# Performance work log

Hardware: AMD Instinct MI355X
Metric: run time of the kernel (lower is better)

## Reference

```python
import math
import jax, jax.numpy as jnp
import numpy as np

HID = 2048      # hidden_size
NH = 16         # num_heads
KD = HID // NH  # key head dim = 128 (even, required by XPOS)
VD = HID        # value_dim (value_factor=1)
VHD = VD // NH  # value head dim
SCALE_BASE = 512
ROPE_BASE = 10000.0
GN_EPS = 1e-5


def _rotate_every_two(x):
    x1 = x[..., ::2]
    x2 = x[..., 1::2]
    return jnp.stack((-x2, x1), axis=-1).reshape(x.shape)


def _dup(a):  # repeat_interleave(x, 2, dim=-1)
    return jnp.repeat(a, 2, axis=-1)


def _xpos_apply(x, pos, inv_freq, xpos_scale, downscale):
    # x: [B, H, S, KD], pos: [B, S]
    posf = pos.astype(jnp.float32)
    angles = posf[:, :, None] * inv_freq[None, None, :]          # [B, S, KD/2]
    sin = _dup(jnp.sin(angles))[:, None]                          # [B, 1, S, KD]
    cos = _dup(jnp.cos(angles))[:, None]
    scale = xpos_scale[None, None, :] ** (posf[:, :, None] / SCALE_BASE)
    if downscale:
        scale = 1.0 / scale
    scale = _dup(scale)[:, None]                                  # [B, 1, S, KD]
    return (x * cos + _rotate_every_two(x) * sin) * scale


def setup_inputs() -> dict:
    key = jax.random.key(0)
    ks = jax.random.split(key, 6)
    B, S = 1, 2048
    std = 1.0 / HID
    x = jax.random.normal(ks[0], (B, S, HID), dtype=jnp.float32)
    position_ids = jnp.broadcast_to(jnp.arange(S, dtype=jnp.int64), (B, S))
    Wq = jax.random.normal(ks[1], (HID, HID), dtype=jnp.float32) * std
    Wk = jax.random.normal(ks[2], (HID, HID), dtype=jnp.float32) * std
    Wv = jax.random.normal(ks[3], (HID, VD), dtype=jnp.float32) * std
    Wg = jax.random.normal(ks[4], (HID, VD), dtype=jnp.float32) * std
    Wo = jax.random.normal(ks[5], (VD, HID), dtype=jnp.float32) * std
    gn_weight = jnp.ones((VD,), dtype=jnp.float32)
    gn_bias = jnp.zeros((VD,), dtype=jnp.float32)
    return {"x": x, "position_ids": position_ids, "Wq": Wq, "Wk": Wk,
            "Wv": Wv, "Wg": Wg, "Wo": Wo,
            "gn_weight": gn_weight, "gn_bias": gn_bias}


def reference(x, position_ids, Wq, Wk, Wv, Wg, Wo, gn_weight, gn_bias):
    B, S, _ = x.shape
    # XPOS / multiscale-decay buffers (deterministic, as in XPOSRelativePosition)
    inv_freq = 1.0 / (ROPE_BASE ** (jnp.arange(0, KD, 2, dtype=jnp.float32) / KD))
    xpos_scale = (jnp.arange(0, KD, 2, dtype=jnp.float32) + 0.4 * KD) / (1.4 * KD)
    gamma = 1.0 - jnp.exp(jnp.linspace(math.log(1.0 / 32), math.log(1.0 / 512), NH))
    log_gamma = jnp.log(gamma)                                    # [NH]

    # projections -> [B, H, S, d]
    q = (x @ Wq).reshape(B, S, NH, KD).transpose(0, 2, 1, 3)
    k = (x @ Wk).reshape(B, S, NH, KD).transpose(0, 2, 1, 3)
    v = (x @ Wv).reshape(B, S, NH, VHD).transpose(0, 2, 1, 3)
    g = x @ Wg                                                    # [B, S, VD]

    q = _xpos_apply(q, position_ids, inv_freq, xpos_scale, downscale=False)
    k = _xpos_apply(k, position_ids, inv_freq, xpos_scale, downscale=True)

    # decay mask: exp(log_gamma * (i-j)) for i>=j else 0   [B, H, S, S]
    relpos = position_ids[:, :, None] - position_ids[:, None, :]  # [B, S, S]
    decay = jnp.exp(log_gamma[None, :, None, None]
                    * jnp.maximum(relpos, 0)[:, None].astype(jnp.float32))
    decay = decay * (relpos >= 0)[:, None].astype(jnp.float32)

    scores = jnp.einsum('bhqd,bhkd->bhqk', q, k) * decay          # [B, H, S, S]
    retained = jnp.einsum('bhqk,bhkv->bhqv', scores, v)           # [B, H, S, VHD]

    # GroupNorm(num_heads, value_dim): normalize each head group per token
    r = retained.transpose(0, 2, 1, 3)                            # [B, S, H, VHD]
    mean = r.mean(axis=-1, keepdims=True)
    var = r.var(axis=-1, keepdims=True)
    rn = (r - mean) * jax.lax.rsqrt(var + GN_EPS)
    rn = rn * gn_weight.reshape(NH, VHD) + gn_bias.reshape(NH, VHD)
    rn = rn.reshape(B, S, VD)

    out = (jax.nn.silu(g) * rn) @ Wo                              # [B, S, HID]
    return out
```

## Files before the change

kernel.cpp:

```cpp
#include <hip/hip_runtime.h>
#include <math.h>

#define S_LEN 2048
#define HIDD  2048
#define NHEAD 16
#define HD    128

#define TILE_SH 4096

typedef __attribute__((ext_vector_type(8))) short short8;
typedef __attribute__((ext_vector_type(4))) float float4v;
typedef unsigned short ushort_t;

static __device__ __forceinline__ ushort_t f2bf(float f) {
    unsigned int u = __float_as_uint(f);
    u += 0x7fff + ((u >> 16) & 1);
    return (ushort_t)(u >> 16);
}
static __device__ __forceinline__ float bf2f(ushort_t s) {
    return __uint_as_float(((unsigned int)s) << 16);
}
__device__ __forceinline__ float silu_f(float x) { return x / (1.f + expf(-x)); }

__device__ __forceinline__ void gl_lds16(const ushort_t* g, short* l) {
    __builtin_amdgcn_global_load_lds((const __attribute__((address_space(1))) void*)g,
                                     (__attribute__((address_space(3))) void*)l, 16, 0, 0);
}

__global__ __launch_bounds__(256)
void split_kernel(const float* __restrict__ in, ushort_t* __restrict__ hi,
                  ushort_t* __restrict__ lo, int n4)
{
    const int i = blockIdx.x * 256 + threadIdx.x;
    if (i >= n4) return;
    const float4 v = ((const float4*)in)[i];
    ushort4 h, l;
    h.x = f2bf(v.x); l.x = f2bf(v.x - bf2f(h.x));
    h.y = f2bf(v.y); l.y = f2bf(v.y - bf2f(h.y));
    h.z = f2bf(v.z); l.z = f2bf(v.z - bf2f(h.z));
    h.w = f2bf(v.w); l.w = f2bf(v.w - bf2f(h.w));
    const int row = i >> 9, c4 = (i & 511) * 4;
    const size_t off = ((size_t)((row >> 7) * 64 + (c4 >> 5))) * TILE_SH
                     + (row & 127) * 32 + (c4 & 31);
    *(ushort4*)&hi[off] = h;
    *(ushort4*)&lo[off] = l;
}

__global__ __launch_bounds__(256)
void addp_kernel(float* __restrict__ out, const float* __restrict__ p, int n4)
{
    const int i = blockIdx.x * 256 + threadIdx.x;
    if (i >= n4) return;
    float4 a = ((const float4*)out)[i];
    const float4 b = ((const float4*)p)[i];
    a.x += b.x; a.y += b.y; a.z += b.z; a.w += b.w;
    ((float4*)out)[i] = a;
}

__global__ __launch_bounds__(256)
void split_transpose(const float* __restrict__ W, ushort_t* __restrict__ Thi,
                     ushort_t* __restrict__ Tlo)
{
    __shared__ float t[64][65];
    const int k0 = blockIdx.y * 64, n0 = blockIdx.x * 64;
    const int tx = threadIdx.x & 15, ty = threadIdx.x >> 4;
    #pragma unroll
    for (int it = 0; it < 4; it++) {
        const int k = ty + it * 16;
        const float4 v = *(const float4*)&W[(size_t)(k0 + k) * HIDD + n0 + tx * 4];
        t[k][tx * 4 + 0] = v.x; t[k][tx * 4 + 1] = v.y;
        t[k][tx * 4 + 2] = v.z; t[k][tx * 4 + 3] = v.w;
    }
    __syncthreads();
    #pragma unroll
    for (int it = 0; it < 4; it++) {
        const int n = ty + it * 16;
        ushort4 h, l; float a;
        a = t[tx * 4 + 0][n]; h.x = f2bf(a); l.x = f2bf(a - bf2f(h.x));
        a = t[tx * 4 + 1][n]; h.y = f2bf(a); l.y = f2bf(a - bf2f(h.y));
        a = t[tx * 4 + 2][n]; h.z = f2bf(a); l.z = f2bf(a - bf2f(h.z));
        a = t[tx * 4 + 3][n]; h.w = f2bf(a); l.w = f2bf(a - bf2f(h.w));
        const int nn_ = n0 + n, kk_ = k0 + tx * 4;
        const size_t off = ((size_t)((nn_ >> 7) * 64 + (kk_ >> 5))) * TILE_SH
                         + (nn_ & 127) * 32 + (kk_ & 31);
        *(ushort4*)&Thi[off] = h;
        *(ushort4*)&Tlo[off] = l;
    }
}

template<int MODE>
__global__ __launch_bounds__(256, 2)
void mfma_gemm(const ushort_t* __restrict__ Ahi, const ushort_t* __restrict__ Alo,
               const ushort_t* __restrict__ WT, const int* __restrict__ pos_ids,
               ushort_t* __restrict__ qhi, ushort_t* __restrict__ qlo,
               ushort_t* __restrict__ khi, ushort_t* __restrict__ klo,
               ushort_t* __restrict__ vThi, ushort_t* __restrict__ vTlo,
               float* __restrict__ gbuf, float* __restrict__ outC)
{
    __shared__ __align__(16) short sm[32768];

    const int tid = threadIdx.x;
    const int w = tid >> 6, L = tid & 63;
    const int qd = L >> 4, lc = L & 15;
    const int lin = blockIdx.x;
    int n0, m0, kh = 0;
    if (MODE == 0) {
        n0 = (((lin & 7) << 3) + ((lin >> 3) & 7)) << 7;
        m0 = (lin >> 6) << 7;
    } else {
        n0 = (lin & 15) << 7;
        m0 = ((lin >> 4) & 15) << 7;
        kh = lin >> 8;
    }
    const size_t PL = (size_t)HIDD * HIDD;

    int sel, nn;
    const ushort_t *Bhi, *Blo;
    if (MODE == 0) {
        sel = n0 >> 11; nn = n0 & 2047;
        Bhi = WT + (size_t)sel * 2 * PL; Blo = Bhi + PL;
    } else {
        sel = -1; nn = n0;
        Bhi = WT; Blo = WT + PL;
    }

    const ushort_t* pbase = (w == 0) ? Ahi : (w == 1) ? Alo : (w == 2) ? Bhi : Blo;
    const int rt = ((w < 2) ? m0 : nn) >> 7;
    const int lsw = ((L >> 2) * 32) + (((L & 3) ^ ((L >> 2) & 3)) * 8);
    const ushort_t* tb0 = pbase + (size_t)rt * 64 * TILE_SH + lsw;

    const int wm = (w & 1) * 64, wn = (w >> 1) * 64;
    const int sx = (qd ^ (lc & 3)) * 8;
    int aoff[4], boff[4];
    #pragma unroll
    for (int i = 0; i < 4; i++) aoff[i] = (wm + i * 16 + lc) * 32 + sx;
    #pragma unroll
    for (int j = 0; j < 4; j++) boff[j] = (wn + j * 16 + lc) * 32 + sx;

    float4v acc[4][4];
    #pragma unroll
    for (int i = 0; i < 4; i++)
        #pragma unroll
        for (int j = 0; j < 4; j++)
            #pragma unroll
            for (int r = 0; r < 4; r++) acc[i][j][r] = 0.f;

    const int kt0 = (MODE == 1) ? kh * 32 : 0;
    const int kt1 = (MODE == 1) ? kt0 + 32 : 64;

    {
        const ushort_t* g = tb0 + (size_t)kt0 * TILE_SH;
        #pragma unroll
        for (int t = 0; t < 8; t++)
            gl_lds16(g + t * 512, sm + w * 4096 + t * 512);
        asm volatile("s_waitcnt vmcnt(0)" ::: "memory");
        __builtin_amdgcn_s_barrier();
        __builtin_amdgcn_sched_barrier(0);
    }

    int cur = 0;
    for (int kt = kt0; kt < kt1; kt++) {
        const short* cb = sm + (cur << 14);
        short* nb = sm + ((cur ^ 1) << 14);
        if (kt + 1 < kt1) {
            const ushort_t* g = tb0 + (size_t)(kt + 1) * TILE_SH;
            #pragma unroll
            for (int t = 0; t < 8; t++)
                gl_lds16(g + t * 512, nb + w * 4096 + t * 512);
        }

        short8 bhf[4], blf[4];
        #pragma unroll
        for (int j = 0; j < 4; j++) {
            bhf[j] = *(const short8*)(cb + 8192  + boff[j]);
            blf[j] = *(const short8*)(cb + 12288 + boff[j]);
        }
        #pragma unroll
        for (int i = 0; i < 4; i++) {
            const short8 ahf = *(const short8*)(cb + aoff[i]);
            const short8 alf = *(const short8*)(cb + 4096 + aoff[i]);
            #pragma unroll
            for (int j = 0; j < 4; j++) {
                acc[i][j] = __builtin_amdgcn_mfma_f32_16x16x32_bf16(ahf, bhf[j], acc[i][j], 0, 0, 0);
                acc[i][j] = __builtin_amdgcn_mfma_f32_16x16x32_bf16(alf, bhf[j], acc[i][j], 0, 0, 0);
                acc[i][j] = __builtin_amdgcn_mfma_f32_16x16x32_bf16(ahf, blf[j], acc[i][j], 0, 0, 0);
            }
        }

        asm volatile("s_waitcnt vmcnt(0)" ::: "memory");
        __builtin_amdgcn_s_barrier();
        __builtin_amdgcn_sched_barrier(0);
        cur ^= 1;
    }

    float* ob = (float*)sm;
    const int half = w & 1;
    const int head = nn >> 7;

    #pragma unroll
    for (int i = 0; i < 4; i++) {
        #pragma unroll
        for (int j = 0; j < 4; j++)
            #pragma unroll
            for (int r = 0; r < 4; r++)
                ob[(half * 16 + qd * 4 + r) * 132 + wn + j * 16 + lc] = acc[i][j][r];
        __syncthreads();

        if (MODE == 1 || sel == 3) {
            float* dst = (MODE == 1) ? (kh ? gbuf : outC) : gbuf;
            #pragma unroll
            for (int p = 0; p < 4; p++) {
                const int row = p * 8 + (tid >> 5);
                const int c = (tid & 31) * 4;
                const int grow = m0 + (row >> 4) * 64 + i * 16 + (row & 15);
                const float4 vv = *(const float4*)&ob[row * 132 + c];
                *(float4*)&dst[(size_t)grow * HIDD + nn + c] = vv;
            }
        } else if (sel == 2) {
            const int d = tid >> 1, hs = tid & 1;
            const int sbase = m0 + hs * 64 + i * 16;
            short8 h0, h1, l0, l1;
            #pragma unroll
            for (int sp = 0; sp < 8; sp++) {
                float a = ob[(hs * 16 + sp) * 132 + d];
                ushort_t hb = f2bf(a);
                h0[sp] = (short)hb; l0[sp] = (short)f2bf(a - bf2f(hb));
                a = ob[(hs * 16 + 8 + sp) * 132 + d];
                hb = f2bf(a);
                h1[sp] = (short)hb; l1[sp] = (short)f2bf(a - bf2f(hb));
            }
            ushort_t* dh = vThi + ((size_t)head * HD + d) * S_LEN + sbase;
            ushort_t* dl = vTlo + ((size_t)head * HD + d) * S_LEN + sbase;
            *(short8*)dh = h0; *(short8*)(dh + 8) = h1;
            *(short8*)dl = l0; *(short8*)(dl + 8) = l1;
        } else {
            const float sgn = (sel == 0) ? 1.f : -1.f;
            ushort_t* dhb = (sel == 0) ? qhi : khi;
            ushort_t* dlb = (sel == 0) ? qlo : klo;
            #pragma unroll
            for (int p = 0; p < 2; p++) {
                const int row = p * 16 + (tid >> 4);
                const int c8 = (tid & 15) * 8;
                const int grow = m0 + (row >> 4) * 64 + i * 16 + (row & 15);
                const float pos = (float)pos_ids[grow];
                const float pe = sgn * pos * (1.f / 512.f);
                short8 hv, lv;
                #pragma unroll
                for (int pp = 0; pp < 4; pp++) {
                    const int d = c8 + pp * 2;
                    const float v0 = ob[row * 132 + d], v1 = ob[row * 132 + d + 1];
                    const float invf = exp2f(-(float)d * (13.28771238f / 128.f));
                    float s, c_; sincosf(pos * invf, &s, &c_);
                    const float scl = exp2f(log2f(((float)d + 51.2f) * (1.f / 179.2f)) * pe);
                    const float e0 = (v0 * c_ - v1 * s) * scl;
                    const float e1 = (v1 * c_ + v0 * s) * scl;
                    const ushort_t h0 = f2bf(e0), h1 = f2bf(e1);
                    hv[pp * 2] = (short)h0;  hv[pp * 2 + 1] = (short)h1;
                    lv[pp * 2] = (short)f2bf(e0 - bf2f(h0));
                    lv[pp * 2 + 1] = (short)f2bf(e1 - bf2f(h1));
                }
                *(short8*)&dhb[((size_t)head * S_LEN + grow) * HD + c8] = hv;
                *(short8*)&dlb[((size_t)head * S_LEN + grow) * HD + c8] = lv;
            }
        }
        __syncthreads();
    }
}

#define KROW 136
#define VROW 40
#define KH_  0
#define KL_  (32 * KROW)
#define VH_  (2 * 32 * KROW)
#define VL_  (VH_ + 128 * VROW)
#define PH_  (VH_ + 2 * 128 * VROW)
#define PLO_ (PH_ + 64 * VROW)
#define YH_  8704
#define YL_  (YH_ + 64 * KROW)
__global__ __launch_bounds__(256, 2)
void retention2(const ushort_t* __restrict__ qhi, const ushort_t* __restrict__ qlo,
                const ushort_t* __restrict__ khi, const ushort_t* __restrict__ klo,
                const ushort_t* __restrict__ vThi, const ushort_t* __restrict__ vTlo,
                const float* __restrict__ gbuf, const float* __restrict__ gnw,
                const float* __restrict__ gnb,
                ushort_t* __restrict__ yhi, ushort_t* __restrict__ ylo)
{
    __shared__ __align__(16) short sm[26112];

    const int h = blockIdx.y;
    const int qb = (gridDim.x - 1) - blockIdx.x;
    const int r0 = qb * 64;
    const int tid = threadIdx.x;
    const int w = tid >> 6, L = tid & 63;
    const int qd = L >> 4, lc = L & 15;

    const float e = -3.4657359f + (float)h * ((-6.2383246f + 3.4657359f) / 15.f);
    const float lg2g = logf(1.f - expf(e)) * 1.44269504f;

    short8 qfh[4], qfl[4];
    {
        const size_t qb0 = ((size_t)h * S_LEN + r0 + w * 16 + lc) * HD + qd * 8;
        #pragma unroll
        for (int ks = 0; ks < 4; ks++) {
            qfh[ks] = *(const short8*)(qhi + qb0 + ks * 32);
            qfl[ks] = *(const short8*)(qlo + qb0 + ks * 32);
        }
    }

    float4v osum[2][4];
    #pragma unroll
    for (int mt = 0; mt < 2; mt++)
        #pragma unroll
        for (int j = 0; j < 4; j++)
            #pragma unroll
            for (int r = 0; r < 4; r++) osum[mt][j][r] = 0.f;

    const int qh_ = w >> 1, vh_ = w & 1;
    const int nch = (r0 + 64) / 32;

    for (int ch = 0; ch < nch; ch++) {
        const int kg0 = ch * 32;
        #pragma unroll
        for (int t = 0; t < 4; t++) {
            const int c = t * 256 + tid;
            const int p = c >> 9, r = (c >> 4) & 31, qq = c & 15;
            const ushort_t* src = (p ? klo : khi) + ((size_t)h * S_LEN + kg0 + r) * HD + qq * 8;
            *(short8*)(sm + (p ? KL_ : KH_) + r * KROW + qq * 8) = *(const short8*)src;
        }
        #pragma unroll
        for (int t = 0; t < 4; t++) {
            const int c = t * 256 + tid;
            const int p = c >> 9, r = (c >> 2) & 127, qq = c & 3;
            const ushort_t* src = (p ? vTlo : vThi) + ((size_t)h * HD + r) * S_LEN + kg0 + qq * 8;
            *(short8*)(sm + (p ? VL_ : VH_) + r * VROW + qq * 8) = *(const short8*)src;
        }
        __syncthreads();

        float4v sacc[2];
        #pragma unroll
        for (int j = 0; j < 2; j++)
            #pragma unroll
            for (int r = 0; r < 4; r++) sacc[j][r] = 0.f;
        #pragma unroll
        for (int ks = 0; ks < 4; ks++) {
            #pragma unroll
            for (int j = 0; j < 2; j++) {
                const short8 bh = *(const short8*)(sm + KH_ + (j * 16 + lc) * KROW + ks * 32 + qd * 8);
                const short8 bl = *(const short8*)(sm + KL_ + (j * 16 + lc) * KROW + ks * 32 + qd * 8);
                sacc[j] = __builtin_amdgcn_mfma_f32_16x16x32_bf16(qfh[ks], bh, sacc[j], 0, 0, 0);
                sacc[j] = __builtin_amdgcn_mfma_f32_16x16x32_bf16(qfl[ks], bh, sacc[j], 0, 0, 0);
                sacc[j] = __builtin_amdgcn_mfma_f32_16x16x32_bf16(qfh[ks], bl, sacc[j], 0, 0, 0);
            }
        }
        #pragma unroll
        for (int j = 0; j < 2; j++)
            #pragma unroll
            for (int r = 0; r < 4; r++) {
                const int dq = (r0 + w * 16 + qd * 4 + r) - (kg0 + j * 16 + lc);
                const float p = (dq >= 0) ? sacc[j][r] * exp2f(lg2g * (float)dq) : 0.f;
                const ushort_t hb = f2bf(p);
                const int off = (w * 16 + qd * 4 + r) * VROW + j * 16 + lc;
                sm[PH_ + off]  = (short)hb;
                sm[PLO_ + off] = (short)f2bf(p - bf2f(hb));
            }
        __syncthreads();

        #pragma unroll
        for (int mt = 0; mt < 2; mt++) {
            const short8 pfh = *(const short8*)(sm + PH_  + (qh_ * 32 + mt * 16 + lc) * VROW + qd * 8);
            const short8 pfl = *(const short8*)(sm + PLO_ + (qh_ * 32 + mt * 16 + lc) * VROW + qd * 8);
            #pragma unroll
            for (int j = 0; j < 4; j++) {
                const short8 vfh = *(const short8*)(sm + VH_ + (vh_ * 64 + j * 16 + lc) * VROW + qd * 8);
                const short8 vfl = *(const short8*)(sm + VL_ + (vh_ * 64 + j * 16 + lc) * VROW + qd * 8);
                osum[mt][j] = __builtin_amdgcn_mfma_f32_16x16x32_bf16(pfh, vfh, osum[mt][j], 0, 0, 0);
                osum[mt][j] = __builtin_amdgcn_mfma_f32_16x16x32_bf16(pfl, vfh, osum[mt][j], 0, 0, 0);
                osum[mt][j] = __builtin_amdgcn_mfma_f32_16x16x32_bf16(pfh, vfl, osum[mt][j], 0, 0, 0);
            }
        }
        __syncthreads();
    }

    float* fr = (float*)sm;
    #pragma unroll
    for (int mt = 0; mt < 2; mt++)
        #pragma unroll
        for (int r = 0; r < 4; r++) {
            float s1 = 0.f, s2 = 0.f;
            #pragma unroll
            for (int j = 0; j < 4; j++) { const float v = osum[mt][j][r]; s1 += v; s2 += v * v; }
            const int row = qh_ * 32 + mt * 16 + qd * 4 + r;
            fr[row * 32 + vh_ * 16 + lc] = s1;
            fr[2048 + row * 32 + vh_ * 16 + lc] = s2;
        }
    __syncthreads();
    if (tid < 64) {
        float s1 = 0.f, s2 = 0.f;
        #pragma unroll
        for (int t = 0; t < 32; t++) { s1 += fr[tid * 32 + t]; s2 += fr[2048 + tid * 32 + t]; }
        const float mean = s1 * (1.f / 128.f);
        const float var  = s2 * (1.f / 128.f) - mean * mean;
        fr[4096 + tid] = mean;
        fr[4160 + tid] = 1.f / sqrtf(var + 1e-5f);
    }
    __syncthreads();

    #pragma unroll
    for (int mt = 0; mt < 2; mt++)
        #pragma unroll
        for (int r = 0; r < 4; r++) {
            const int row = qh_ * 32 + mt * 16 + qd * 4 + r;
            const float mean = fr[4096 + row], inv = fr[4160 + row];
            const int grow = r0 + row;
            #pragma unroll
            for (int j = 0; j < 4; j++) {
                const int col = vh_ * 64 + j * 16 + lc;
                const float gv = gbuf[(size_t)grow * HIDD + h * HD + col];
                const float o = ((osum[mt][j][r] - mean) * inv * gnw[h * HD + col]
                                 + gnb[h * HD + col]) * silu_f(gv);
                const ushort_t hb = f2bf(o);
                sm[YH_ + row * KROW + col] = (short)hb;
                sm[YL_ + row * KROW + col] = (short)f2bf(o - bf2f(hb));
            }
        }
    __syncthreads();
    {
        const int r_ = tid >> 2, cs = (tid & 3) * 32;
        const int grow = r0 + r_;
        const size_t tb = ((size_t)((grow >> 7) * 64 + h * 4 + (tid & 3))) * TILE_SH
                        + (grow & 127) * 32;
        #pragma unroll
        for (int c8 = 0; c8 < 4; c8++) {
            *(short8*)(yhi + tb + c8 * 8) = *(const short8*)(sm + YH_ + r_ * KROW + cs + c8 * 8);
            *(short8*)(ylo + tb + c8 * 8) = *(const short8*)(sm + YL_ + r_ * KROW + cs + c8 * 8);
        }
    }
}

extern "C" void kernel_launch(void* const* d_in, const int* in_sizes, int n_in,
                              void* d_out, int out_size, void* d_ws, size_t ws_size,
                              hipStream_t stream) {
    const float* x   = (const float*)d_in[0];
    const int*   pid = (const int*)d_in[1];
    const float* W[5] = {(const float*)d_in[2], (const float*)d_in[3], (const float*)d_in[4],
                         (const float*)d_in[5], (const float*)d_in[6]};
    const float* gnw = (const float*)d_in[7];
    const float* gnb = (const float*)d_in[8];
    float* out = (float*)d_out;
    (void)in_sizes; (void)n_in; (void)out_size; (void)ws_size;

    const size_t PL = (size_t)HIDD * HIDD;

    ushort_t* wt   = (ushort_t*)d_ws;
    ushort_t* xhi  = wt + 10 * PL;
    ushort_t* xlo  = xhi + PL;
    ushort_t* qhi_ = xlo + PL;
    ushort_t* qlo_ = qhi_ + PL;
    ushort_t* khi_ = qlo_ + PL;
    ushort_t* klo_ = khi_ + PL;
    ushort_t* vThi = klo_ + PL;
    ushort_t* vTlo = vThi + PL;
    float*    gbuf = (float*)(vTlo + PL);
    ushort_t* yhi  = (ushort_t*)(gbuf + PL);
    ushort_t* ylo  = yhi + PL;
    float*    p1   = (float*)xhi;

    split_kernel<<<(int)(PL / 4 / 256), 256, 0, stream>>>(x, xhi, xlo, (int)(PL / 4));
    for (int m = 0; m < 5; m++)
        split_transpose<<<dim3(32, 32), 256, 0, stream>>>(W[m], wt + (size_t)m * 2 * PL,
                                                          wt + (size_t)m * 2 * PL + PL);

    mfma_gemm<0><<<1024, 256, 0, stream>>>(xhi, xlo, wt, pid,
        qhi_, qlo_, khi_, klo_, vThi, vTlo, gbuf, nullptr);

    retention2<<<dim3(32, 16), 256, 0, stream>>>(qhi_, qlo_, khi_, klo_, vThi, vTlo,
        gbuf, gnw, gnb, yhi, ylo);

    mfma_gemm<1><<<512, 256, 0, stream>>>(yhi, ylo, wt + 8 * PL, pid,
        nullptr, nullptr, nullptr, nullptr, nullptr, nullptr, p1, out);

    addp_kernel<<<(int)(PL / 4 / 256), 256, 0, stream>>>(out, p1, (int)(PL / 4));
}
```

Before: 535.5 us.

## Widen GEMM tiles to 128x256 and split output GEMM K four ways

The split-bf16 MFMA GEMM now computes 128x256 output tiles per block instead of 128x128, so each A tile loaded into LDS is reused across twice as many columns. The grid drops to 512 blocks for both GEMMs, and the output projection splits K into four parts instead of two to keep the block count. The extra partials are summed by an extended add kernel. The A-side load is reordered after a barrier so it can reuse a single buffer, which trades some copy overlap and more LDS and registers (32 accumulators) for fewer redundant loads.

```diff
diff --git a/kernel.cpp b/kernel.cpp
--- a/kernel.cpp
+++ b/kernel.cpp
@@ -52,8 +52,13 @@
     const int i = blockIdx.x * 256 + threadIdx.x;
     if (i >= n4) return;
     float4 a = ((const float4*)out)[i];
-    const float4 b = ((const float4*)p)[i];
-    a.x += b.x; a.y += b.y; a.z += b.z; a.w += b.w;
+    const float4 b0 = ((const float4*)p)[i];
+    const float4 b1 = ((const float4*)p)[i + n4];
+    const float4 b2 = ((const float4*)p)[i + 2 * n4];
+    a.x += b0.x + b1.x + b2.x;
+    a.y += b0.y + b1.y + b2.y;
+    a.z += b0.z + b1.z + b2.z;
+    a.w += b0.w + b1.w + b2.w;
     ((float4*)out)[i] = a;
 }
 
@@ -97,7 +102,7 @@
                ushort_t* __restrict__ vThi, ushort_t* __restrict__ vTlo,
                float* __restrict__ gbuf, float* __restrict__ outC)
 {
-    __shared__ __align__(16) short sm[32768];
+    __shared__ __align__(16) short sm[40960];
 
     const int tid = threadIdx.x;
     const int w = tid >> 6, L = tid & 63;
@@ -105,12 +110,12 @@
     const int lin = blockIdx.x;
     int n0, m0, kh = 0;
     if (MODE == 0) {
-        n0 = (((lin & 7) << 3) + ((lin >> 3) & 7)) << 7;
-        m0 = (lin >> 6) << 7;
+        n0 = (((lin & 7) << 2) + ((lin >> 3) & 3)) << 8;
+        m0 = (lin >> 5) << 7;
     } else {
-        n0 = (lin & 15) << 7;
-        m0 = ((lin >> 4) & 15) << 7;
-        kh = lin >> 8;
+        n0 = (lin & 7) << 8;
+        m0 = ((lin >> 3) & 15) << 7;
+        kh = lin >> 7;
     }
     const size_t PL = (size_t)HIDD * HIDD;
 
@@ -126,33 +131,40 @@
 
     const ushort_t* pbase = (w == 0) ? Ahi : (w == 1) ? Alo : (w == 2) ? Bhi : Blo;
     const int rt = ((w < 2) ? m0 : nn) >> 7;
-    const int lsw = ((L >> 2) * 32) + (((L & 3) ^ ((L >> 2) & 3)) * 8);
-    const ushort_t* tb0 = pbase + (size_t)rt * 64 * TILE_SH + lsw;
-
-    const int wm = (w & 1) * 64, wn = (w >> 1) * 64;
-    const int sx = (qd ^ (lc & 3)) * 8;
-    int aoff[4], boff[4];
-    #pragma unroll
-    for (int i = 0; i < 4; i++) aoff[i] = (wm + i * 16 + lc) * 32 + sx;
-    #pragma unroll
-    for (int j = 0; j < 4; j++) boff[j] = (wn + j * 16 + lc) * 32 + sx;
-
-    float4v acc[4][4];
+    const ushort_t* tb0 = pbase + (size_t)rt * 64 * TILE_SH + L * 8;
+
+    const int wm = (w & 1) * 64;
+    const int wnh = w >> 1;
+    int aoff[4], boff[8];
+    #pragma unroll
+    for (int i = 0; i < 4; i++) aoff[i] = (wm + i * 16 + lc) * 32 + qd * 8;
+    #pragma unroll
+    for (int jj = 0; jj < 8; jj++) boff[jj] = (jj * 16 + lc) * 32 + qd * 8;
+
+    float4v acc[4][8];
     #pragma unroll
     for (int i = 0; i < 4; i++)
         #pragma unroll
-        for (int j = 0; j < 4; j++)
-            #pragma unroll
-            for (int r = 0; r < 4; r++) acc[i][j][r] = 0.f;
-
-    const int kt0 = (MODE == 1) ? kh * 32 : 0;
-    const int kt1 = (MODE == 1) ? kt0 + 32 : 64;
+        for (int jj = 0; jj < 8; jj++)
+            #pragma unroll
+            for (int r = 0; r < 4; r++) acc[i][jj][r] = 0.f;
+
+    const int kt0 = (MODE == 1) ? kh * 16 : 0;
+    const int kt1 = (MODE == 1) ? kt0 + 16 : 64;
 
     {
         const ushort_t* g = tb0 + (size_t)kt0 * TILE_SH;
-        #pragma unroll
-        for (int t = 0; t < 8; t++)
-            gl_lds16(g + t * 512, sm + w * 4096 + t * 512);
+        if (w < 2) {
+            short* d = sm + w * 4096;
+            #pragma unroll
+            for (int t = 0; t < 8; t++) gl_lds16(g + t * 512, d + t * 512);
+        } else {
+            short* d = sm + 8192 + (w - 2) * 8192;
+            #pragma unroll
+            for (int t = 0; t < 8; t++) gl_lds16(g + t * 512, d + t * 512);
+            #pragma unroll
+            for (int t = 0; t < 8; t++) gl_lds16(g + 64 * TILE_SH + t * 512, d + 4096 + t * 512);
+        }
         asm volatile("s_waitcnt vmcnt(0)" ::: "memory");
         __builtin_amdgcn_s_barrier();
         __builtin_amdgcn_sched_barrier(0);
@@ -160,33 +172,49 @@
 
     int cur = 0;
     for (int kt = kt0; kt < kt1; kt++) {
-        const short* cb = sm + (cur << 14);
-        short* nb = sm + ((cur ^ 1) << 14);
-        if (kt + 1 < kt1) {
+        if (w >= 2 && kt + 1 < kt1) {
             const ushort_t* g = tb0 + (size_t)(kt + 1) * TILE_SH;
-            #pragma unroll
-            for (int t = 0; t < 8; t++)
-                gl_lds16(g + t * 512, nb + w * 4096 + t * 512);
-        }
-
-        short8 bhf[4], blf[4];
-        #pragma unroll
-        for (int j = 0; j < 4; j++) {
-            bhf[j] = *(const short8*)(cb + 8192  + boff[j]);
-            blf[j] = *(const short8*)(cb + 12288 + boff[j]);
-        }
+            short* d = sm + 8192 + ((cur ^ 1) * 16384) + (w - 2) * 8192;
+            #pragma unroll
+            for (int t = 0; t < 8; t++) gl_lds16(g + t * 512, d + t * 512);
+            #pragma unroll
+            for (int t = 0; t < 8; t++) gl_lds16(g + 64 * TILE_SH + t * 512, d + 4096 + t * 512);
+        }
+
+        short8 ah[4], al[4];
         #pragma unroll
         for (int i = 0; i < 4; i++) {
-            const short8 ahf = *(const short8*)(cb + aoff[i]);
-            const short8 alf = *(const short8*)(cb + 4096 + aoff[i]);
+            ah[i] = *(const short8*)(sm + aoff[i]);
+            al[i] = *(const short8*)(sm + 4096 + aoff[i]);
+        }
+        const short* bb = sm + 8192 + cur * 16384 + wnh * 4096;
+        #pragma unroll
+        for (int jh = 0; jh < 2; jh++) {
+            short8 bh[4], bl[4];
             #pragma unroll
             for (int j = 0; j < 4; j++) {
-                acc[i][j] = __builtin_amdgcn_mfma_f32_16x16x32_bf16(ahf, bhf[j], acc[i][j], 0, 0, 0);
-                acc[i][j] = __builtin_amdgcn_mfma_f32_16x16x32_bf16(alf, bhf[j], acc[i][j], 0, 0, 0);
-                acc[i][j] = __builtin_amdgcn_mfma_f32_16x16x32_bf16(ahf, blf[j], acc[i][j], 0, 0, 0);
-            }
-        }
-
+                bh[j] = *(const short8*)(bb + boff[jh * 4 + j]);
+                bl[j] = *(const short8*)(bb + 8192 + boff[jh * 4 + j]);
+            }
+            #pragma unroll
+            for (int i = 0; i < 4; i++)
+                #pragma unroll
+                for (int j = 0; j < 4; j++) {
+                    acc[i][jh * 4 + j] = __builtin_amdgcn_mfma_f32_16x16x32_bf16(ah[i], bh[j], acc[i][jh * 4 + j], 0, 0, 0);
+                    acc[i][jh * 4 + j] = __builtin_amdgcn_mfma_f32_16x16x32_bf16(al[i], bh[j], acc[i][jh * 4 + j], 0, 0, 0);
+                    acc[i][jh * 4 + j] = __builtin_amdgcn_mfma_f32_16x16x32_bf16(ah[i], bl[j], acc[i][jh * 4 + j], 0, 0, 0);
+                }
+        }
+
+        asm volatile("s_waitcnt lgkmcnt(0)" ::: "memory");
+        __builtin_amdgcn_s_barrier();
+        __builtin_amdgcn_sched_barrier(0);
+        if (w < 2 && kt + 1 < kt1) {
+            const ushort_t* g = tb0 + (size_t)(kt + 1) * TILE_SH;
+            short* d = sm + w * 4096;
+            #pragma unroll
+            for (int t = 0; t < 8; t++) gl_lds16(g + t * 512, d + t * 512);
+        }
         asm volatile("s_waitcnt vmcnt(0)" ::: "memory");
         __builtin_amdgcn_s_barrier();
         __builtin_amdgcn_sched_barrier(0);
@@ -194,73 +222,82 @@
     }
 
     float* ob = (float*)sm;
-    const int half = w & 1;
-    const int head = nn >> 7;
+    const int mh = w & 1;
+    const int headb = nn >> 7;
 
     #pragma unroll
     for (int i = 0; i < 4; i++) {
         #pragma unroll
-        for (int j = 0; j < 4; j++)
+        for (int jj = 0; jj < 8; jj++)
             #pragma unroll
             for (int r = 0; r < 4; r++)
-                ob[(half * 16 + qd * 4 + r) * 132 + wn + j * 16 + lc] = acc[i][j][r];
+                ob[(mh * 16 + qd * 4 + r) * 260 + wnh * 128 + jj * 16 + lc] = acc[i][jj][r];
         __syncthreads();
 
         if (MODE == 1 || sel == 3) {
-            float* dst = (MODE == 1) ? (kh ? gbuf : outC) : gbuf;
-            #pragma unroll
-            for (int p = 0; p < 4; p++) {
-                const int row = p * 8 + (tid >> 5);
-                const int c = (tid & 31) * 4;
+            float* dst = (MODE == 1) ? ((kh == 0) ? outC : gbuf + (size_t)(kh - 1) * PL)
+                                     : gbuf;
+            #pragma unroll
+            for (int p = 0; p < 8; p++) {
+                const int row = p * 4 + (tid >> 6);
+                const int c = (tid & 63) * 4;
                 const int grow = m0 + (row >> 4) * 64 + i * 16 + (row & 15);
-                const float4 vv = *(const float4*)&ob[row * 132 + c];
+                const float4 vv = *(const float4*)&ob[row * 260 + c];
                 *(float4*)&dst[(size_t)grow * HIDD + nn + c] = vv;
             }
         } else if (sel == 2) {
             const int d = tid >> 1, hs = tid & 1;
             const int sbase = m0 + hs * 64 + i * 16;
-            short8 h0, h1, l0, l1;
-            #pragma unroll
-            for (int sp = 0; sp < 8; sp++) {
-                float a = ob[(hs * 16 + sp) * 132 + d];
-                ushort_t hb = f2bf(a);
-                h0[sp] = (short)hb; l0[sp] = (short)f2bf(a - bf2f(hb));
-                a = ob[(hs * 16 + 8 + sp) * 132 + d];
-                hb = f2bf(a);
-                h1[sp] = (short)hb; l1[sp] = (short)f2bf(a - bf2f(hb));
-            }
-            ushort_t* dh = vThi + ((size_t)head * HD + d) * S_LEN + sbase;
-            ushort_t* dl = vTlo + ((size_t)head * HD + d) * S_LEN + sbase;
-            *(short8*)dh = h0; *(short8*)(dh + 8) = h1;
-            *(short8*)dl = l0; *(short8*)(dl + 8) = l1;
+            #pragma unroll
+            for (int nh = 0; nh < 2; nh++) {
+                short8 h0, h1, l0, l1;
+                #pragma unroll
+                for (int sp = 0; sp < 8; sp++) {
+                    float a = ob[(hs * 16 + sp) * 260 + nh * 128 + d];
+                    ushort_t hb = f2bf(a);
+                    h0[sp] = (short)hb; l0[sp] = (short)f2bf(a - bf2f(hb));
+                    a = ob[(hs * 16 + 8 + sp) * 260 + nh * 128 + d];
+                    hb = f2bf(a);
+                    h1[sp] = (short)hb; l1[sp] = (short)f2bf(a - bf2f(hb));
+                }
+                ushort_t* dh = vThi + ((size_t)(headb + nh) * HD + d) * S_LEN + sbase;
+                ushort_t* dl = vTlo + ((size_t)(headb + nh) * HD + d) * S_LEN + sbase;
+                *(short8*)dh = h0; *(short8*)(dh + 8) = h1;
+                *(short8*)dl = l0; *(short8*)(dl + 8) = l1;
+            }
         } else {
             const float sgn = (sel == 0) ? 1.f : -1.f;
             ushort_t* dhb = (sel == 0) ? qhi : khi;
             ushort_t* dlb = (sel == 0) ? qlo : klo;
             #pragma unroll
-            for (int p = 0; p < 2; p++) {
-                const int row = p * 16 + (tid >> 4);
-                const int c8 = (tid & 15) * 8;
-                const int grow = m0 + (row >> 4) * 64 + i * 16 + (row & 15);
-                const float pos = (float)pos_ids[grow];
-                const float pe = sgn * pos * (1.f / 512.f);
-                short8 hv, lv;
+            for (int nh = 0; nh < 2; nh++) {
+                const int head = headb + nh;
                 #pragma unroll
-                for (int pp = 0; pp < 4; pp++) {
-                    const int d = c8 + pp * 2;
-                    const float v0 = ob[row * 132 + d], v1 = ob[row * 132 + d + 1];
-                    const float invf = exp2f(-(float)d * (13.28771238f / 128.f));
-                    float s, c_; sincosf(pos * invf, &s, &c_);
-                    const float scl = exp2f(log2f(((float)d + 51.2f) * (1.f / 179.2f)) * pe);
-                    const float e0 = (v0 * c_ - v1 * s) * scl;
-                    const float e1 = (v1 * c_ + v0 * s) * scl;
-                    const ushort_t h0 = f2bf(e0), h1 = f2bf(e1);
-                    hv[pp * 2] = (short)h0;  hv[pp * 2 + 1] = (short)h1;
-                    lv[pp * 2] = (short)f2bf(e0 - bf2f(h0));
-                    lv[pp * 2 + 1] = (short)f2bf(e1 - bf2f(h1));
+                for (int p = 0; p < 2; p++) {
+                    const int row = p * 16 + (tid >> 4);
+                    const int c8 = (tid & 15) * 8;
+                    const int grow = m0 + (row >> 4) * 64 + i * 16 + (row & 15);
+                    const float pos = (float)pos_ids[grow];
+                    const float pe = sgn * pos * (1.f / 512.f);
+                    short8 hv, lv;
+                    #pragma unroll
+                    for (int pp = 0; pp < 4; pp++) {
+                        const int d = c8 + pp * 2;
+                        const float v0 = ob[row * 260 + nh * 128 + d];
+                        const float v1 = ob[row * 260 + nh * 128 + d + 1];
+                        const float invf = exp2f(-(float)d * (13.28771238f / 128.f));
+                        float s, c_; sincosf(pos * invf, &s, &c_);
+                        const float scl = exp2f(log2f(((float)d + 51.2f) * (1.f / 179.2f)) * pe);
+                        const float e0 = (v0 * c_ - v1 * s) * scl;
+                        const float e1 = (v1 * c_ + v0 * s) * scl;
+                        const ushort_t h0 = f2bf(e0), h1 = f2bf(e1);
+                        hv[pp * 2] = (short)h0;  hv[pp * 2 + 1] = (short)h1;
+                        lv[pp * 2] = (short)f2bf(e0 - bf2f(h0));
+                        lv[pp * 2 + 1] = (short)f2bf(e1 - bf2f(h1));
+                    }
+                    *(short8*)&dhb[((size_t)head * S_LEN + grow) * HD + c8] = hv;
+                    *(short8*)&dlb[((size_t)head * S_LEN + grow) * HD + c8] = lv;
                 }
-                *(short8*)&dhb[((size_t)head * S_LEN + grow) * HD + c8] = hv;
-                *(short8*)&dlb[((size_t)head * S_LEN + grow) * HD + c8] = lv;
             }
         }
         __syncthreads();
@@ -463,21 +500,21 @@
     float*    gbuf = (float*)(vTlo + PL);
     ushort_t* yhi  = (ushort_t*)(gbuf + PL);
     ushort_t* ylo  = yhi + PL;
-    float*    p1   = (float*)xhi;
+    float*    pb   = (float*)xhi;
 
     split_kernel<<<(int)(PL / 4 / 256), 256, 0, stream>>>(x, xhi, xlo, (int)(PL / 4));
     for (int m = 0; m < 5; m++)
         split_transpose<<<dim3(32, 32), 256, 0, stream>>>(W[m], wt + (size_t)m * 2 * PL,
                                                           wt + (size_t)m * 2 * PL + PL);
 
-    mfma_gemm<0><<<1024, 256, 0, stream>>>(xhi, xlo, wt, pid,
+    mfma_gemm<0><<<512, 256, 0, stream>>>(xhi, xlo, wt, pid,
         qhi_, qlo_, khi_, klo_, vThi, vTlo, gbuf, nullptr);
 
     retention2<<<dim3(32, 16), 256, 0, stream>>>(qhi_, qlo_, khi_, klo_, vThi, vTlo,
         gbuf, gnw, gnb, yhi, ylo);
 
     mfma_gemm<1><<<512, 256, 0, stream>>>(yhi, ylo, wt + 8 * PL, pid,
-        nullptr, nullptr, nullptr, nullptr, nullptr, nullptr, p1, out);
-
-    addp_kernel<<<(int)(PL / 4 / 256), 256, 0, stream>>>(out, p1, (int)(PL / 4));
-}
+        nullptr, nullptr, nullptr, nullptr, nullptr, nullptr, pb, out);
+
+    addp_kernel<<<(int)(PL / 4 / 256), 256, 0, stream>>>(out, pb, (int)(PL / 4));
+}
```

Result: slower. 579.2 us (+8.2%).

## Single-buffer LDS in the projection GEMM and drop the bank-conflict swizzle

Applied to the files above, without the earlier changes.

For MODE 0 (the QKV/G projection), the double-buffered prefetch loop becomes a single-buffered load, sync, compute, sync loop. This halves that kernel's shared memory, which could allow more resident blocks. The XOR swizzle on LDS load and read offsets is removed in both modes and replaced by a linear layout, which simplifies address math. The cost is that global-to-LDS loads no longer overlap with MFMA work, and LDS bank conflicts are likely to return on the fragment reads.

```diff
diff --git a/kernel.cpp b/kernel.cpp
--- a/kernel.cpp
+++ b/kernel.cpp
@@ -97,7 +97,7 @@
                ushort_t* __restrict__ vThi, ushort_t* __restrict__ vTlo,
                float* __restrict__ gbuf, float* __restrict__ outC)
 {
-    __shared__ __align__(16) short sm[32768];
+    __shared__ __align__(16) short sm[(MODE == 1) ? 32768 : 16384];
 
     const int tid = threadIdx.x;
     const int w = tid >> 6, L = tid & 63;
@@ -126,16 +126,14 @@
 
     const ushort_t* pbase = (w == 0) ? Ahi : (w == 1) ? Alo : (w == 2) ? Bhi : Blo;
     const int rt = ((w < 2) ? m0 : nn) >> 7;
-    const int lsw = ((L >> 2) * 32) + (((L & 3) ^ ((L >> 2) & 3)) * 8);
-    const ushort_t* tb0 = pbase + (size_t)rt * 64 * TILE_SH + lsw;
+    const ushort_t* tb0 = pbase + (size_t)rt * 64 * TILE_SH + L * 8;
 
     const int wm = (w & 1) * 64, wn = (w >> 1) * 64;
-    const int sx = (qd ^ (lc & 3)) * 8;
     int aoff[4], boff[4];
     #pragma unroll
-    for (int i = 0; i < 4; i++) aoff[i] = (wm + i * 16 + lc) * 32 + sx;
-    #pragma unroll
-    for (int j = 0; j < 4; j++) boff[j] = (wn + j * 16 + lc) * 32 + sx;
+    for (int i = 0; i < 4; i++) aoff[i] = (wm + i * 16 + lc) * 32 + qd * 8;
+    #pragma unroll
+    for (int j = 0; j < 4; j++) boff[j] = (wn + j * 16 + lc) * 32 + qd * 8;
 
     float4v acc[4][4];
     #pragma unroll
@@ -148,49 +146,76 @@
     const int kt0 = (MODE == 1) ? kh * 32 : 0;
     const int kt1 = (MODE == 1) ? kt0 + 32 : 64;
 
-    {
-        const ushort_t* g = tb0 + (size_t)kt0 * TILE_SH;
-        #pragma unroll
-        for (int t = 0; t < 8; t++)
-            gl_lds16(g + t * 512, sm + w * 4096 + t * 512);
-        asm volatile("s_waitcnt vmcnt(0)" ::: "memory");
-        __builtin_amdgcn_s_barrier();
-        __builtin_amdgcn_sched_barrier(0);
-    }
-
-    int cur = 0;
-    for (int kt = kt0; kt < kt1; kt++) {
-        const short* cb = sm + (cur << 14);
-        short* nb = sm + ((cur ^ 1) << 14);
-        if (kt + 1 < kt1) {
-            const ushort_t* g = tb0 + (size_t)(kt + 1) * TILE_SH;
+    if (MODE == 0) {
+        short* ldsw = sm + w * 4096;
+        for (int kt = kt0; kt < kt1; kt++) {
+            const ushort_t* g = tb0 + (size_t)kt * TILE_SH;
             #pragma unroll
             for (int t = 0; t < 8; t++)
-                gl_lds16(g + t * 512, nb + w * 4096 + t * 512);
-        }
-
-        short8 bhf[4], blf[4];
-        #pragma unroll
-        for (int j = 0; j < 4; j++) {
-            bhf[j] = *(const short8*)(cb + 8192  + boff[j]);
-            blf[j] = *(const short8*)(cb + 12288 + boff[j]);
-        }
-        #pragma unroll
-        for (int i = 0; i < 4; i++) {
-            const short8 ahf = *(const short8*)(cb + aoff[i]);
-            const short8 alf = *(const short8*)(cb + 4096 + aoff[i]);
+                gl_lds16(g + t * 512, ldsw + t * 512);
+            __syncthreads();
+
+            short8 bhf[4], blf[4];
             #pragma unroll
             for (int j = 0; j < 4; j++) {
-                acc[i][j] = __builtin_amdgcn_mfma_f32_16x16x32_bf16(ahf, bhf[j], acc[i][j], 0, 0, 0);
-                acc[i][j] = __builtin_amdgcn_mfma_f32_16x16x32_bf16(alf, bhf[j], acc[i][j], 0, 0, 0);
-                acc[i][j] = __builtin_amdgcn_mfma_f32_16x16x32_bf16(ahf, blf[j], acc[i][j], 0, 0, 0);
-            }
-        }
-
-        asm volatile("s_waitcnt vmcnt(0)" ::: "memory");
-        __builtin_amdgcn_s_barrier();
-        __builtin_amdgcn_sched_barrier(0);
-        cur ^= 1;
+                bhf[j] = *(const short8*)(sm + 8192  + boff[j]);
+                blf[j] = *(const short8*)(sm + 12288 + boff[j]);
+            }
+            #pragma unroll
+            for (int i = 0; i < 4; i++) {
+                const short8 ahf = *(const short8*)(sm + aoff[i]);
+                const short8 alf = *(const short8*)(sm + 4096 + aoff[i]);
+                #pragma unroll
+                for (int j = 0; j < 4; j++) {
+                    acc[i][j] = __builtin_amdgcn_mfma_f32_16x16x32_bf16(ahf, bhf[j], acc[i][j], 0, 0, 0);
+                    acc[i][j] = __builtin_amdgcn_mfma_f32_16x16x32_bf16(alf, bhf[j], acc[i][j], 0, 0, 0);
+                    acc[i][j] = __builtin_amdgcn_mfma_f32_16x16x32_bf16(ahf, blf[j], acc[i][j], 0, 0, 0);
+                }
+            }
+            __syncthreads();
+        }
+    } else {
+        {
+            const ushort_t* g = tb0 + (size_t)kt0 * TILE_SH;
+            #pragma unroll
+            for (int t = 0; t < 8; t++)
+                gl_lds16(g + t * 512, sm + w * 4096 + t * 512);
+            asm volatile("s_waitcnt vmcnt(0)" ::: "memory");
+            __builtin_amdgcn_s_barrier();
+            __builtin_amdgcn_sched_barrier(0);
+        }
+        int cur = 0;
+        for (int kt = kt0; kt < kt1; kt++) {
+            const short* cb = sm + (cur << 14);
+            short* nb = sm + ((cur ^ 1) << 14);
+            if (kt + 1 < kt1) {
+                const ushort_t* g = tb0 + (size_t)(kt + 1) * TILE_SH;
+                #pragma unroll
+                for (int t = 0; t < 8; t++)
+                    gl_lds16(g + t * 512, nb + w * 4096 + t * 512);
+            }
+            short8 bhf[4], blf[4];
+            #pragma unroll
+            for (int j = 0; j < 4; j++) {
+                bhf[j] = *(const short8*)(cb + 8192  + boff[j]);
+                blf[j] = *(const short8*)(cb + 12288 + boff[j]);
+            }
+            #pragma unroll
+            for (int i = 0; i < 4; i++) {
+                const short8 ahf = *(const short8*)(cb + aoff[i]);
+                const short8 alf = *(const short8*)(cb + 4096 + aoff[i]);
+                #pragma unroll
+                for (int j = 0; j < 4; j++) {
+                    acc[i][j] = __builtin_amdgcn_mfma_f32_16x16x32_bf16(ahf, bhf[j], acc[i][j], 0, 0, 0);
+                    acc[i][j] = __builtin_amdgcn_mfma_f32_16x16x32_bf16(alf, bhf[j], acc[i][j], 0, 0, 0);
+                    acc[i][j] = __builtin_amdgcn_mfma_f32_16x16x32_bf16(ahf, blf[j], acc[i][j], 0, 0, 0);
+                }
+            }
+            asm volatile("s_waitcnt vmcnt(0)" ::: "memory");
+            __builtin_amdgcn_s_barrier();
+            __builtin_amdgcn_sched_barrier(0);
+            cur ^= 1;
+        }
     }
 
     float* ob = (float*)sm;
```

New measurement: 559.1 us. 4.4% more time.
